# Optimization experiments

Measured on AMD Instinct MI355X. Metric: run time of the kernel, lower is better.

Reference implementation:

```python
import jax, jax.numpy as jnp
import numpy as np

H, D, KV, S, PAST, BS, NB = 32, 128, 8, 128, 8064, 128, 128
T = PAST + S          # total context = 8192
NBLK = T // BS        # logical blocks used = 64
NEG = jnp.float32(-1e30)


def setup_inputs() -> dict:
    key = jax.random.key(0)
    ks = jax.random.split(key, 6)
    q = jax.random.normal(ks[0], (1, H, S, D), jnp.float32)
    k = jax.random.normal(ks[1], (1, KV, S, D), jnp.float32)
    v = jax.random.normal(ks[2], (1, KV, S, D), jnp.float32)
    pk = jax.random.normal(ks[3], (NB, KV, BS, D), jnp.float32)
    pv = jax.random.normal(ks[4], (NB, KV, BS, D), jnp.float32)
    # block table: 64 logical blocks mapped to distinct physical blocks (paged indirection)
    bt = jax.random.permutation(ks[5], NB)[:NBLK].astype(jnp.int32)
    return dict(
        query_state=q, key_state=k, value_state=v,
        attn_mask=jnp.ones((1,), jnp.float32),  # unused: causal prefill path (use_attention_mask=False)
        past_key_state=pk, past_value_state=pv,
        seq_position=PAST,
        scale=jnp.float32(1.0 / np.sqrt(D)),
        block_tables=bt, block_size=BS,
    )


def reference(query_state, key_state, value_state, attn_mask,
              past_key_state, past_value_state, seq_position, scale,
              block_tables, block_size):
    # phase == 'prefill', use_attention_mask=False -> paged_causal_attn_prefill
    kvh = past_key_state.shape[1]
    s_new = query_state.shape[2]
    total = seq_position + s_new  # static python int

    # --- append new K/V into the paged cache at positions [seq_position, total) ---
    pos_new = seq_position + jnp.arange(s_new)
    blk = block_tables[pos_new // block_size]
    off = pos_new % block_size
    k_new = jnp.transpose(key_state[0], (1, 0, 2))    # [S, KV, D]
    v_new = jnp.transpose(value_state[0], (1, 0, 2))
    kc = past_key_state.at[blk, :, off, :].set(k_new)
    vc = past_value_state.at[blk, :, off, :].set(v_new)

    # --- gather the full context [0, total) through the block table ---
    pos = jnp.arange(total)
    blk_a = block_tables[pos // block_size]
    off_a = pos % block_size
    K = kc[blk_a, :, off_a, :]   # [T, KV, D]
    V = vc[blk_a, :, off_a, :]

    # --- grouped-query causal attention ---
    g = query_state.shape[1] // kvh
    q = query_state.reshape(kvh, g, s_new, -1)                 # [KV, G, S, D]
    scores = jnp.einsum('kgsd,tkd->kgst', q, K) * scale        # [KV, G, S, T]
    causal = pos[None, :] <= (seq_position + jnp.arange(s_new))[:, None]  # [S, T]
    scores = jnp.where(causal[None, None], scores, NEG)
    probs = jax.nn.softmax(scores, axis=-1)
    out = jnp.einsum('kgst,tkd->kgsd', probs, V)               # [KV, G, S, D]

    h = kvh * g
    out = out.reshape(1, h, s_new, -1)                         # [1, H, S, D]
    out = jnp.transpose(out, (0, 2, 1, 3)).reshape(1, s_new, h * out.shape[-1])
    return out
```

## Files before the change

kernel.cpp:

```cpp
#include <hip/hip_runtime.h>
#include <hip/hip_bf16.h>


typedef unsigned short u16;
typedef unsigned int u32;
typedef __bf16 bf16x8 __attribute__((ext_vector_type(8)));
typedef float f32x16 __attribute__((ext_vector_type(16)));
typedef float f32x4 __attribute__((ext_vector_type(4)));
typedef u32 u32x4 __attribute__((ext_vector_type(4)));
typedef u32 u32x2 __attribute__((ext_vector_type(2)));

#define NHEAD 32
#define DH 128
#define NKV 8
#define SQ 128
#define PAST_T 8064
#define TOTAL_T 8192
#define BK 32
#define KSTR 136
#define VSTR 34
#define WSPP (16384 + 256)
#define MSUB 17.3123405f

__device__ __forceinline__ u32 pk2f(float lo, float hi) {
  union {
    __hip_bfloat162 b;
    u32 u;
  } cv;
  cv.b = __float22bfloat162_rn(make_float2(lo, hi));
  return cv.u;
}

template <int NPART>
__global__ __launch_bounds__(256, 2) void flash_part(
    const float* __restrict__ q, const float* __restrict__ knew,
    const float* __restrict__ vnew, const float* __restrict__ pk,
    const float* __restrict__ pv, const int* __restrict__ btab,
    const float* __restrict__ scp, float* __restrict__ ws) {
  constexpr int CHUNK = TOTAL_T / NPART;
  constexpr int NITER = CHUNK / BK;
  __shared__ __attribute__((aligned(16))) u16 k_s[2 * BK * KSTR];
  __shared__ __attribute__((aligned(16))) u16 vt_s[2 * DH * VSTR];
  __shared__ int bt_s[64];

  const int bid = blockIdx.x;
  const int r = bid & 31, u = bid >> 5;
  const int g = r >> 3;
  const int idx = u * 8 + (r & 7);
  const int kv = idx & 7;
  const int p = idx >> 3;
  const int h = kv * 4 + g;

  const int tid = threadIdx.x;
  const int lane = tid & 63, w = tid >> 6;
  const int l31 = lane & 31, grp = lane >> 5;
  const int pstart = p * CHUNK;

  if (tid < 64) bt_s[tid] = btab[tid];
  const float qs = scp[0] * 1.44269504f;

  u32x4 qf[8];
  {
    const float* qp = q + ((size_t)(h * SQ + w * 32 + l31)) * DH;
#pragma unroll
    for (int st = 0; st < 8; ++st) {
      const f32x4 a = *(const f32x4*)(qp + st * 16 + grp * 8);
      const f32x4 b = *(const f32x4*)(qp + st * 16 + grp * 8 + 4);
      u32x4 f;
      f[0] = pk2f(a[0] * qs, a[1] * qs);
      f[1] = pk2f(a[2] * qs, a[3] * qs);
      f[2] = pk2f(b[0] * qs, b[1] * qs);
      f[3] = pk2f(b[2] * qs, b[3] * qs);
      qf[st] = f;
    }
  }

  f32x16 oacc[4];
#pragma unroll
  for (int i = 0; i < 4; ++i)
#pragma unroll
    for (int rr = 0; rr < 16; ++rr) oacc[i][rr] = 0.0f;
  float l_acc = 0.0f;

  __syncthreads();

  f32x4 kr[4];
  f32x4 v0[2], v1[2];
  const int kc4 = (tid & 31) * 4;
  const int ktrow = tid >> 5;
  const int va4 = (tid & 31) * 4;
  const int vtp = tid >> 5;

  auto load_tile = [&](int it) {
    const int t0 = pstart + it * BK;
    const float *sk, *sv;
    if (t0 < PAST_T) {
      const size_t boff =
          (((size_t)bt_s[t0 >> 7] * NKV + kv) * 128 + (t0 & 127)) * (size_t)DH;
      sk = pk + boff;
      sv = pv + boff;
    } else {
      const size_t noff = ((size_t)kv * SQ + (t0 - PAST_T)) * (size_t)DH;
      sk = knew + noff;
      sv = vnew + noff;
    }
#pragma unroll
    for (int j = 0; j < 4; ++j)
      kr[j] = *(const f32x4*)(sk + (size_t)(j * 8 + ktrow) * DH + kc4);
#pragma unroll
    for (int rr = 0; rr < 2; ++rr) {
      const int t = 2 * (vtp + rr * 8);
      v0[rr] = *(const f32x4*)(sv + (size_t)t * DH + va4);
      v1[rr] = *(const f32x4*)(sv + (size_t)(t + 1) * DH + va4);
    }
  };
  auto store_tile = [&](int buf) {
    u16* ks = k_s + buf * (BK * KSTR);
    u16* vs = vt_s + buf * (DH * VSTR);
#pragma unroll
    for (int j = 0; j < 4; ++j) {
      u32x2 pw;
      pw[0] = pk2f(kr[j][0], kr[j][1]);
      pw[1] = pk2f(kr[j][2], kr[j][3]);
      *(u32x2*)&ks[(j * 8 + ktrow) * KSTR + kc4] = pw;
    }
#pragma unroll
    for (int rr = 0; rr < 2; ++rr) {
      const int t = 2 * (vtp + rr * 8);
#pragma unroll
      for (int j = 0; j < 4; ++j)
        *(u32*)&vs[(va4 + j) * VSTR + t] = pk2f(v0[rr][j], v1[rr][j]);
    }
  };

  load_tile(0);
  store_tile(0);
  __syncthreads();

  for (int it = 0; it < NITER; ++it) {
    const int buf = it & 1;
    if (it + 1 < NITER) load_tile(it + 1);

    const u16* ks = k_s + buf * (BK * KSTR);
    const u16* vs = vt_s + buf * (DH * VSTR);
    const int t0 = pstart + it * BK;

    f32x16 sacc;
#pragma unroll
    for (int rr = 0; rr < 16; ++rr) sacc[rr] = 0.0f;
#pragma unroll
    for (int st = 0; st < 8; ++st) {
      const u32x4 kf = *(const u32x4*)&ks[l31 * KSTR + st * 16 + grp * 8];
      sacc = __builtin_amdgcn_mfma_f32_32x32x16_bf16(
          __builtin_bit_cast(bf16x8, kf), __builtin_bit_cast(bf16x8, qf[st]),
          sacc, 0, 0, 0);
    }

    const int qcol = w * 32 + l31;
    float pr[16];
    if (t0 > PAST_T - BK) {
#pragma unroll
      for (int rr = 0; rr < 16; ++rr) {
        const int trow = (rr & 3) + 8 * (rr >> 2) + 4 * grp;
        const float e = exp2f(sacc[rr] - MSUB);
        pr[rr] = ((t0 + trow - PAST_T) > qcol) ? 0.0f : e;
      }
    } else {
#pragma unroll
      for (int rr = 0; rr < 16; ++rr) pr[rr] = exp2f(sacc[rr] - MSUB);
    }
    float rs = 0.0f;
#pragma unroll
    for (int rr = 0; rr < 16; ++rr) rs += pr[rr];
    l_acc += rs;

    u32 pkk[8], xch[8];
#pragma unroll
    for (int j = 0; j < 8; ++j) pkk[j] = pk2f(pr[2 * j], pr[2 * j + 1]);
#pragma unroll
    for (int j = 0; j < 8; ++j) xch[j] = (u32)__shfl_xor((int)pkk[j], 32, 64);

    u32x4 pf1, pf2;
    pf1[0] = grp ? xch[2] : pkk[0];
    pf1[1] = grp ? xch[3] : pkk[1];
    pf1[2] = grp ? pkk[2] : xch[0];
    pf1[3] = grp ? pkk[3] : xch[1];
    pf2[0] = grp ? xch[6] : pkk[4];
    pf2[1] = grp ? xch[7] : pkk[5];
    pf2[2] = grp ? pkk[6] : xch[4];
    pf2[3] = grp ? pkk[7] : xch[5];

#pragma unroll
    for (int dt = 0; dt < 4; ++dt) {
      const int dd = dt * 32 + l31;
      const u16* vp = &vs[dd * VSTR + grp * 8];
      u32x4 av;
      av[0] = *(const u32*)(vp + 0);
      av[1] = *(const u32*)(vp + 2);
      av[2] = *(const u32*)(vp + 4);
      av[3] = *(const u32*)(vp + 6);
      oacc[dt] = __builtin_amdgcn_mfma_f32_32x32x16_bf16(
          __builtin_bit_cast(bf16x8, av), __builtin_bit_cast(bf16x8, pf1),
          oacc[dt], 0, 0, 0);
      const u16* vq = vp + 16;
      u32x4 bv;
      bv[0] = *(const u32*)(vq + 0);
      bv[1] = *(const u32*)(vq + 2);
      bv[2] = *(const u32*)(vq + 4);
      bv[3] = *(const u32*)(vq + 6);
      oacc[dt] = __builtin_amdgcn_mfma_f32_32x32x16_bf16(
          __builtin_bit_cast(bf16x8, bv), __builtin_bit_cast(bf16x8, pf2),
          oacc[dt], 0, 0, 0);
    }

    if (it + 1 < NITER) store_tile(buf ^ 1);
    __syncthreads();
  }

  float* wsp = ws + (size_t)(h * NPART + p) * WSPP;
#pragma unroll
  for (int dt = 0; dt < 4; ++dt)
#pragma unroll
    for (int rr = 0; rr < 16; ++rr) {
      const int dd = dt * 32 + (rr & 3) + 8 * (rr >> 2) + 4 * grp;
      wsp[dd * 128 + w * 32 + l31] = oacc[dt][rr];
    }
  const float l_tot = l_acc + __shfl_xor(l_acc, 32, 64);
  if (grp == 0) wsp[16384 + w * 32 + l31] = l_tot;
}

template <int NPART>
__global__ __launch_bounds__(256, 2) void combine_out(
    const float* __restrict__ ws, float* __restrict__ out) {
  __shared__ float rden_s[128];
  __shared__ float tr_s[128 * 9];

  const int dblk = blockIdx.x;
  const int h = blockIdx.y;
  const int tid = threadIdx.x;
  const float* base = ws + (size_t)h * NPART * WSPP;

  if (tid < 128) {
    float denom = 0.0f;
#pragma unroll
    for (int pp = 0; pp < NPART; ++pp)
      denom += base[(size_t)pp * WSPP + 16384 + tid];
    rden_s[tid] = 1.0f / denom;
  }
  __syncthreads();

  const int sq = tid & 31, dr = tid >> 5;
  {
    const int d = dblk * 8 + dr;
    float a[4] = {0.0f, 0.0f, 0.0f, 0.0f};
#pragma unroll
    for (int pp = 0; pp < NPART; ++pp) {
      const f32x4 o = *(const f32x4*)&base[(size_t)pp * WSPP + d * 128 + sq * 4];
#pragma unroll
      for (int j = 0; j < 4; ++j) a[j] += o[j];
    }
#pragma unroll
    for (int j = 0; j < 4; ++j)
      tr_s[(sq * 4 + j) * 9 + dr] = a[j] * rden_s[sq * 4 + j];
  }
  __syncthreads();

  {
    const int s = tid >> 1, dl0 = (tid & 1) * 4;
    f32x4 o;
#pragma unroll
    for (int j = 0; j < 4; ++j) o[j] = tr_s[s * 9 + dl0 + j];
    *(f32x4*)(out + (size_t)s * (NHEAD * DH) + h * DH + dblk * 8 + dl0) = o;
  }
}

extern "C" void kernel_launch(void* const* d_in, const int* in_sizes, int n_in,
                              void* d_out, int out_size, void* d_ws,
                              size_t ws_size, hipStream_t stream) {
  const float* q = (const float*)d_in[0];
  const float* knew = (const float*)d_in[1];
  const float* vnew = (const float*)d_in[2];
  const float* pk = (const float*)d_in[4];
  const float* pv = (const float*)d_in[5];
  const float* scp = (const float*)d_in[7];
  const int* btab = (const int*)d_in[8];
  float* ws = (float*)d_ws;
  float* out = (float*)d_out;

  const size_t need16 = (size_t)NHEAD * 16 * WSPP * sizeof(float);
  const size_t need8 = (size_t)NHEAD * 8 * WSPP * sizeof(float);
  if (ws_size >= need16) {
    flash_part<16><<<dim3(32 * 16), 256, 0, stream>>>(q, knew, vnew, pk, pv,
                                                      btab, scp, ws);
    combine_out<16><<<dim3(16, NHEAD), 256, 0, stream>>>(ws, out);
  } else if (ws_size >= need8) {
    flash_part<8><<<dim3(32 * 8), 256, 0, stream>>>(q, knew, vnew, pk, pv,
                                                    btab, scp, ws);
    combine_out<8><<<dim3(16, NHEAD), 256, 0, stream>>>(ws, out);
  }
}
```

Baseline: 176.2 us.

## Deepen K/V prefetch to two register stages ahead of compute

Global K/V tile loads now go into two alternating register stages, so loads are issued two iterations ahead of use instead of one. The main loop is unrolled by two to keep the register-stage and LDS-buffer roles static. The goal is to hide more global memory latency behind MFMA work, at the cost of doubling the prefetch registers, which may reduce occupancy under launch_bounds(256,2) or cause spills.

```diff
diff --git a/kernel.cpp b/kernel.cpp
--- a/kernel.cpp
+++ b/kernel.cpp
@@ -39,6 +39,7 @@
     const float* __restrict__ scp, float* __restrict__ ws) {
   constexpr int CHUNK = TOTAL_T / NPART;
   constexpr int NITER = CHUNK / BK;
+  static_assert(NITER >= 4 && (NITER & 1) == 0, "pipeline needs even NITER>=4");
   __shared__ __attribute__((aligned(16))) u16 k_s[2 * BK * KSTR];
   __shared__ __attribute__((aligned(16))) u16 vt_s[2 * DH * VSTR];
   __shared__ int bt_s[64];
@@ -84,14 +85,17 @@
 
   __syncthreads();
 
-  f32x4 kr[4];
-  f32x4 v0[2], v1[2];
+  struct Stage {
+    f32x4 kr[4];
+    f32x4 v0[2], v1[2];
+  };
+  Stage sA, sB;
   const int kc4 = (tid & 31) * 4;
   const int ktrow = tid >> 5;
   const int va4 = (tid & 31) * 4;
   const int vtp = tid >> 5;
 
-  auto load_tile = [&](int it) {
+  auto load_tile = [&](Stage& s, int it) {
     const int t0 = pstart + it * BK;
     const float *sk, *sv;
     if (t0 < PAST_T) {
@@ -106,22 +110,22 @@
     }
 #pragma unroll
     for (int j = 0; j < 4; ++j)
-      kr[j] = *(const f32x4*)(sk + (size_t)(j * 8 + ktrow) * DH + kc4);
+      s.kr[j] = *(const f32x4*)(sk + (size_t)(j * 8 + ktrow) * DH + kc4);
 #pragma unroll
     for (int rr = 0; rr < 2; ++rr) {
       const int t = 2 * (vtp + rr * 8);
-      v0[rr] = *(const f32x4*)(sv + (size_t)t * DH + va4);
-      v1[rr] = *(const f32x4*)(sv + (size_t)(t + 1) * DH + va4);
+      s.v0[rr] = *(const f32x4*)(sv + (size_t)t * DH + va4);
+      s.v1[rr] = *(const f32x4*)(sv + (size_t)(t + 1) * DH + va4);
     }
   };
-  auto store_tile = [&](int buf) {
+  auto store_tile = [&](int buf, const Stage& s) {
     u16* ks = k_s + buf * (BK * KSTR);
     u16* vs = vt_s + buf * (DH * VSTR);
 #pragma unroll
     for (int j = 0; j < 4; ++j) {
       u32x2 pw;
-      pw[0] = pk2f(kr[j][0], kr[j][1]);
-      pw[1] = pk2f(kr[j][2], kr[j][3]);
+      pw[0] = pk2f(s.kr[j][0], s.kr[j][1]);
+      pw[1] = pk2f(s.kr[j][2], s.kr[j][3]);
       *(u32x2*)&ks[(j * 8 + ktrow) * KSTR + kc4] = pw;
     }
 #pragma unroll
@@ -129,18 +133,11 @@
       const int t = 2 * (vtp + rr * 8);
 #pragma unroll
       for (int j = 0; j < 4; ++j)
-        *(u32*)&vs[(va4 + j) * VSTR + t] = pk2f(v0[rr][j], v1[rr][j]);
+        *(u32*)&vs[(va4 + j) * VSTR + t] = pk2f(s.v0[rr][j], s.v1[rr][j]);
     }
   };
 
-  load_tile(0);
-  store_tile(0);
-  __syncthreads();
-
-  for (int it = 0; it < NITER; ++it) {
-    const int buf = it & 1;
-    if (it + 1 < NITER) load_tile(it + 1);
-
+  auto compute = [&](int it, int buf) {
     const u16* ks = k_s + buf * (BK * KSTR);
     const u16* vs = vt_s + buf * (DH * VSTR);
     const int t0 = pstart + it * BK;
@@ -212,8 +209,22 @@
           __builtin_bit_cast(bf16x8, bv), __builtin_bit_cast(bf16x8, pf2),
           oacc[dt], 0, 0, 0);
     }
-
-    if (it + 1 < NITER) store_tile(buf ^ 1);
+  };
+
+  load_tile(sA, 0);
+  store_tile(0, sA);
+  load_tile(sA, 1);
+  load_tile(sB, 2);
+  __syncthreads();
+
+  for (int it = 0; it < NITER; it += 2) {
+    compute(it, 0);
+    if (it + 1 < NITER) store_tile(1, sA);
+    if (it + 3 < NITER) load_tile(sA, it + 3);
+    __syncthreads();
+    compute(it + 1, 1);
+    if (it + 2 < NITER) store_tile(0, sB);
+    if (it + 4 < NITER) load_tile(sB, it + 4);
     __syncthreads();
   }
 
```

Measured after the change: 175.6 us. About the same (-0.3%).

## Share each K/V tile between two GQA heads per 512-thread block

Applied to the files above, without the earlier changes.

Each workgroup now runs 8 waves covering two query heads of the same KV group, instead of 4 waves for a single head. Every K/V tile loaded from global memory and converted to bf16 in LDS is reused by twice as many heads. The grid is halved and launch bounds change to 512x1. This cuts redundant global loads and conversion work per head, at the cost of larger workgroups and a barrier that now spans 8 waves.

```diff
diff --git a/kernel.cpp b/kernel.cpp
--- a/kernel.cpp
+++ b/kernel.cpp
@@ -32,7 +32,7 @@
 }
 
 template <int NPART>
-__global__ __launch_bounds__(256, 2) void flash_part(
+__global__ __launch_bounds__(512, 1) void flash_part(
     const float* __restrict__ q, const float* __restrict__ knew,
     const float* __restrict__ vnew, const float* __restrict__ pk,
     const float* __restrict__ pv, const int* __restrict__ btab,
@@ -44,15 +44,17 @@
   __shared__ int bt_s[64];
 
   const int bid = blockIdx.x;
-  const int r = bid & 31, u = bid >> 5;
-  const int g = r >> 3;
-  const int idx = u * 8 + (r & 7);
-  const int kv = idx & 7;
-  const int p = idx >> 3;
-  const int h = kv * 4 + g;
+  const int kv = bid & 7;
+  const int t = bid >> 3;
+  const int p = t % NPART;
+  const int gp = t / NPART;
 
   const int tid = threadIdx.x;
-  const int lane = tid & 63, w = tid >> 6;
+  const int wid = tid >> 6;
+  const int lane = tid & 63;
+  const int g2 = wid & 1;
+  const int w = wid >> 1;
+  const int h = kv * 4 + gp * 2 + g2;
   const int l31 = lane & 31, grp = lane >> 5;
   const int pstart = p * CHUNK;
 
@@ -84,8 +86,7 @@
 
   __syncthreads();
 
-  f32x4 kr[4];
-  f32x4 v0[2], v1[2];
+  f32x4 kr0, kr1, v0, v1;
   const int kc4 = (tid & 31) * 4;
   const int ktrow = tid >> 5;
   const int va4 = (tid & 31) * 4;
@@ -104,33 +105,29 @@
       sk = knew + noff;
       sv = vnew + noff;
     }
-#pragma unroll
-    for (int j = 0; j < 4; ++j)
-      kr[j] = *(const f32x4*)(sk + (size_t)(j * 8 + ktrow) * DH + kc4);
-#pragma unroll
-    for (int rr = 0; rr < 2; ++rr) {
-      const int t = 2 * (vtp + rr * 8);
-      v0[rr] = *(const f32x4*)(sv + (size_t)t * DH + va4);
-      v1[rr] = *(const f32x4*)(sv + (size_t)(t + 1) * DH + va4);
-    }
+    kr0 = *(const f32x4*)(sk + (size_t)ktrow * DH + kc4);
+    kr1 = *(const f32x4*)(sk + (size_t)(ktrow + 16) * DH + kc4);
+    v0 = *(const f32x4*)(sv + (size_t)(2 * vtp) * DH + va4);
+    v1 = *(const f32x4*)(sv + (size_t)(2 * vtp + 1) * DH + va4);
   };
   auto store_tile = [&](int buf) {
     u16* ks = k_s + buf * (BK * KSTR);
     u16* vs = vt_s + buf * (DH * VSTR);
-#pragma unroll
-    for (int j = 0; j < 4; ++j) {
+    {
       u32x2 pw;
-      pw[0] = pk2f(kr[j][0], kr[j][1]);
-      pw[1] = pk2f(kr[j][2], kr[j][3]);
-      *(u32x2*)&ks[(j * 8 + ktrow) * KSTR + kc4] = pw;
-    }
-#pragma unroll
-    for (int rr = 0; rr < 2; ++rr) {
-      const int t = 2 * (vtp + rr * 8);
-#pragma unroll
-      for (int j = 0; j < 4; ++j)
-        *(u32*)&vs[(va4 + j) * VSTR + t] = pk2f(v0[rr][j], v1[rr][j]);
-    }
+      pw[0] = pk2f(kr0[0], kr0[1]);
+      pw[1] = pk2f(kr0[2], kr0[3]);
+      *(u32x2*)&ks[ktrow * KSTR + kc4] = pw;
+    }
+    {
+      u32x2 pw;
+      pw[0] = pk2f(kr1[0], kr1[1]);
+      pw[1] = pk2f(kr1[2], kr1[3]);
+      *(u32x2*)&ks[(ktrow + 16) * KSTR + kc4] = pw;
+    }
+#pragma unroll
+    for (int j = 0; j < 4; ++j)
+      *(u32*)&vs[(va4 + j) * VSTR + 2 * vtp] = pk2f(v0[j], v1[j]);
   };
 
   load_tile(0);
@@ -290,12 +287,12 @@
   const size_t need16 = (size_t)NHEAD * 16 * WSPP * sizeof(float);
   const size_t need8 = (size_t)NHEAD * 8 * WSPP * sizeof(float);
   if (ws_size >= need16) {
-    flash_part<16><<<dim3(32 * 16), 256, 0, stream>>>(q, knew, vnew, pk, pv,
-                                                      btab, scp, ws);
+    flash_part<16><<<dim3(8 * 2 * 16), 512, 0, stream>>>(q, knew, vnew, pk, pv,
+                                                         btab, scp, ws);
     combine_out<16><<<dim3(16, NHEAD), 256, 0, stream>>>(ws, out);
   } else if (ws_size >= need8) {
-    flash_part<8><<<dim3(32 * 8), 256, 0, stream>>>(q, knew, vnew, pk, pv,
-                                                    btab, scp, ws);
+    flash_part<8><<<dim3(8 * 2 * 8), 512, 0, stream>>>(q, knew, vnew, pk, pv,
+                                                       btab, scp, ws);
     combine_out<8><<<dim3(16, NHEAD), 256, 0, stream>>>(ws, out);
   }
 }
```

After: 172.6 us. -2.0%, faster.
